# Kernel optimization log

Hardware: AMD Instinct MI355X
Metric: run time of the kernel (lower is better)

The kernel has to match this reference:

```python
import jax, jax.numpy as jnp
import numpy as np

N_HEAD = 16
N_EMBD = 2048
HEAD_DIM = N_EMBD // N_HEAD


def setup_inputs() -> dict:
    key = jax.random.key(0)
    kx, kqkv, kp = jax.random.split(key, 3)
    B, S = 2, 2048
    x = jax.random.normal(kx, (B, S, N_EMBD), dtype=jnp.float32)
    # torch nn.Linear weights, stored as [out, in]; y = x @ W.T
    scale = 1.0 / np.sqrt(N_EMBD)
    Wqkv = jax.random.uniform(kqkv, (3 * N_EMBD, N_EMBD), dtype=jnp.float32, minval=-scale, maxval=scale)
    Wproj = jax.random.uniform(kp, (N_EMBD, N_EMBD), dtype=jnp.float32, minval=-scale, maxval=scale)
    return {"x": x, "Wqkv": Wqkv, "Wproj": Wproj}


def reference(x, Wqkv, Wproj):
    B, S, E = x.shape
    qkv = x @ Wqkv.T  # [B,S,3E]
    q, k, v = jnp.split(qkv, 3, axis=2)
    # [B,H,S,D]
    q = q.reshape(B, S, N_HEAD, HEAD_DIM).transpose(0, 2, 1, 3)
    k = k.reshape(B, S, N_HEAD, HEAD_DIM).transpose(0, 2, 1, 3)
    v = v.reshape(B, S, N_HEAD, HEAD_DIM).transpose(0, 2, 1, 3)
    scores = jnp.einsum('bhqd,bhkd->bhqk', q, k) / jnp.sqrt(jnp.float32(HEAD_DIM))
    causal = jnp.tril(jnp.ones((S, S), dtype=bool))  # [S,S]
    scores = jnp.where(causal[None, None, :, :], scores, -jnp.inf)
    weights = jax.nn.softmax(scores, axis=-1)
    out = jnp.einsum('bhqk,bhkd->bhqd', weights, v)  # [B,H,S,D]
    out = out.transpose(0, 2, 1, 3).reshape(B, S, E)
    return out @ Wproj.T
```

## Files before the change

kernel.cpp:

```cpp
#include <hip/hip_runtime.h>
#include <cstdint>
#include <cstddef>

typedef __bf16 bf16;
typedef __bf16 bf16x8 __attribute__((ext_vector_type(8)));
typedef float  f32x4  __attribute__((ext_vector_type(4)));

static_assert(sizeof(bf16x8) == 16, "bf16x8 must be 16B");

__device__ __forceinline__ void async_copy16(const bf16* g, bf16* l) {
  __builtin_amdgcn_global_load_lds(
      (__attribute__((address_space(1))) void*)(g),
      (__attribute__((address_space(3))) void*)(l),
      16, 0, 0);
}

__global__ __launch_bounds__(256)
void conv_f32_bf16(const float* __restrict__ s, bf16* __restrict__ d) {
  const size_t i = ((size_t)blockIdx.x * 256 + threadIdx.x) * 8;
  const f32x4 a = *(const f32x4*)(s + i);
  const f32x4 b = *(const f32x4*)(s + i + 4);
  bf16x8 o;
#pragma unroll
  for (int e = 0; e < 4; ++e) { o[e] = (bf16)a[e]; o[4 + e] = (bf16)b[e]; }
  *(bf16x8*)(d + i) = o;
}

template<int AMODE, int CMODE>
__global__ __launch_bounds__(256, 2)
void gemm_bt(const bf16* __restrict__ A, const bf16* __restrict__ W,
             float* __restrict__ Crow, bf16* __restrict__ Cq,
             bf16* __restrict__ Ck, bf16* __restrict__ Cvt,
             int M, int N, int K, int nbase) {
  __shared__ bf16 As[128 * 64];
  __shared__ bf16 Ws[128 * 64];

  const int tid  = threadIdx.x;
  const int wave = tid >> 6;
  const int lane = tid & 63;
  const int quad = lane >> 4;
  const int r    = lane & 15;
  const int m0 = blockIdx.y * 128;
  const int n0 = blockIdx.x * 128;
  const int wm = (wave >> 1) * 64;
  const int wn = (wave & 1) * 64;

  const int lrow   = lane >> 3;
  const int gchunk = (lane & 7) ^ lrow;

  f32x4 acc[4][4] = {};

  for (int k0 = 0; k0 < K; k0 += 64) {
    __syncthreads();
    for (int j = 0; j < 4; ++j) {
      const int rbase = (wave * 4 + j) * 8;
      const int rowA  = m0 + rbase + lrow;
      const bf16* aSrc;
      if constexpr (AMODE == 2) {
        const int b = rowA >> 11, s = rowA & 2047;
        aSrc = A + ((size_t)(b * 16 + (k0 >> 7)) * 2048 + s) * 128
                 + (k0 & 127) + gchunk * 8;
      } else {
        aSrc = A + (size_t)rowA * K + k0 + gchunk * 8;
      }
      async_copy16(aSrc, As + rbase * 64);
      async_copy16(W + (size_t)(n0 + rbase + lrow) * K + k0 + gchunk * 8,
                   Ws + rbase * 64);
    }
    __syncthreads();
    for (int ks = 0; ks < 2; ++ks) {
      bf16x8 af[4], bfv[4];
      for (int i = 0; i < 4; ++i) {
        const int ar = wm + i * 16 + r;
        af[i]  = *(const bf16x8*)(As + ar * 64 + (((ks * 4 + quad) ^ (ar & 7)) * 8));
        const int br = wn + i * 16 + r;
        bfv[i] = *(const bf16x8*)(Ws + br * 64 + (((ks * 4 + quad) ^ (br & 7)) * 8));
      }
      for (int i = 0; i < 4; ++i)
        for (int j = 0; j < 4; ++j)
          acc[i][j] = __builtin_amdgcn_mfma_f32_16x16x32_bf16(af[i], bfv[j], acc[i][j], 0, 0, 0);
    }
  }

  for (int i = 0; i < 4; ++i) {
    const int growb = m0 + wm + i * 16 + quad * 4;
    for (int j = 0; j < 4; ++j) {
      const int gcol = n0 + wn + j * 16 + r;
      for (int rg = 0; rg < 4; ++rg) {
        const int grow = growb + rg;
        if constexpr (CMODE == 1) {
          const int gc = nbase + gcol;
          const int which = gc >> 11;
          const int h = (gc >> 7) & 15;
          const int d = gc & 127;
          const int b = grow >> 11;
          const int s = grow & 2047;
          const bf16 v = (bf16)acc[i][j][rg];
          if (which == 0)
            Cq[(((size_t)b * 16 + h) * 2048 + s) * 128 + d] = v;
          else if (which == 1)
            Ck[(((size_t)b * 16 + h) * 2048 + s) * 128 + d] = v;
          else
            Cvt[(((size_t)b * 16 + h) * 128 + d) * 2048 + s] = v;
        } else {
          Crow[(size_t)grow * N + gcol] = acc[i][j][rg];
        }
      }
    }
  }
}

__global__ __launch_bounds__(256, 2)
void attn_kernel(bf16* __restrict__ Q, const bf16* __restrict__ K,
                 const bf16* __restrict__ Vt, int S) {
  __shared__ bf16 k_lds[64 * 128];
  __shared__ bf16 v_lds[128 * 64];
  __shared__ bf16 p_lds[4][32 * 64];

  const int tid = threadIdx.x, wave = tid >> 6, lane = tid & 63;
  const int quad = lane >> 4, r = lane & 15;
  const int bh = blockIdx.y;
  const int q0 = (gridDim.x - 1 - blockIdx.x) * 128;
  const int qrow0 = q0 + wave * 32;
  bf16* Qh = Q + (size_t)bh * S * 128;
  const bf16* Kh = K + (size_t)bh * S * 128;
  const bf16* Vth = Vt + (size_t)bh * 128 * S;

  bf16x8 qf[2][4];
  for (int mt = 0; mt < 2; ++mt)
    for (int ks = 0; ks < 4; ++ks)
      qf[mt][ks] = *(const bf16x8*)(Qh + (size_t)(qrow0 + mt * 16 + r) * 128 + ks * 32 + quad * 8);

  f32x4 o_acc[2][8] = {};
  f32x4 m_run[2], l_run[2];
  for (int mt = 0; mt < 2; ++mt)
    for (int t = 0; t < 4; ++t) { m_run[mt][t] = -1e30f; l_run[mt][t] = 0.f; }

  const float sc = 0.0883883476483184f * 1.4426950408889634f;
  const int nkv = (q0 + 128) >> 6;

  for (int kt = 0; kt < nkv; ++kt) {
    const int kv0 = kt << 6;
    __syncthreads();
    for (int j = 0; j < 4; ++j) {
      const int lin = j * 256 + tid;
      const int row = lin >> 4;
      const int ch  = lin & 15;
      *(bf16x8*)(k_lds + row * 128 + (ch ^ (row & 7)) * 8) =
          *(const bf16x8*)(Kh + (size_t)(kv0 + row) * 128 + ch * 8);
    }
    for (int j = 0; j < 4; ++j) {
      const int lin = j * 256 + tid;
      const int row = lin >> 3;
      const int c   = lin & 7;
      *(bf16x8*)(v_lds + row * 64 + (c ^ (row & 7)) * 8) =
          *(const bf16x8*)(Vth + (size_t)row * S + kv0 + c * 8);
    }
    __syncthreads();

    if (kv0 <= qrow0 + 31) {
      f32x4 sa[2][4] = {};
      for (int ks = 0; ks < 4; ++ks) {
        bf16x8 kf[4];
        for (int nt = 0; nt < 4; ++nt) {
          const int kr = nt * 16 + r;
          kf[nt] = *(const bf16x8*)(k_lds + kr * 128 + (((ks * 4 + quad) ^ (kr & 7)) * 8));
        }
        for (int mt = 0; mt < 2; ++mt)
          for (int nt = 0; nt < 4; ++nt)
            sa[mt][nt] = __builtin_amdgcn_mfma_f32_16x16x32_bf16(qf[mt][ks], kf[nt], sa[mt][nt], 0, 0, 0);
      }
      if (kv0 + 63 > qrow0) {
        for (int mt = 0; mt < 2; ++mt)
          for (int nt = 0; nt < 4; ++nt) {
            const int col  = kv0 + nt * 16 + r;
            const int rowb = qrow0 + mt * 16 + quad * 4;
            for (int rg = 0; rg < 4; ++rg)
              if (col > rowb + rg) sa[mt][nt][rg] = -1e30f;
          }
      }
      for (int mt = 0; mt < 2; ++mt) {
        f32x4 mx = sa[mt][0];
        for (int nt = 1; nt < 4; ++nt)
          for (int rg = 0; rg < 4; ++rg) mx[rg] = fmaxf(mx[rg], sa[mt][nt][rg]);
        for (int off = 1; off < 16; off <<= 1)
          for (int rg = 0; rg < 4; ++rg) mx[rg] = fmaxf(mx[rg], __shfl_xor(mx[rg], off, 64));
        f32x4 alpha;
        for (int rg = 0; rg < 4; ++rg) {
          const float mnew = fmaxf(m_run[mt][rg], mx[rg]);
          alpha[rg] = exp2f((m_run[mt][rg] - mnew) * sc);
          m_run[mt][rg] = mnew;
        }
        f32x4 rsum = {0.f, 0.f, 0.f, 0.f};
        for (int nt = 0; nt < 4; ++nt)
          for (int rg = 0; rg < 4; ++rg) {
            const float p = exp2f((sa[mt][nt][rg] - m_run[mt][rg]) * sc);
            sa[mt][nt][rg] = p;
            rsum[rg] += p;
          }
        for (int off = 1; off < 16; off <<= 1)
          for (int rg = 0; rg < 4; ++rg) rsum[rg] += __shfl_xor(rsum[rg], off, 64);
        for (int rg = 0; rg < 4; ++rg) l_run[mt][rg] = l_run[mt][rg] * alpha[rg] + rsum[rg];
        for (int nt2 = 0; nt2 < 8; ++nt2)
          for (int rg = 0; rg < 4; ++rg) o_acc[mt][nt2][rg] *= alpha[rg];
        for (int nt = 0; nt < 4; ++nt)
          for (int rg = 0; rg < 4; ++rg) {
            const int prow = mt * 16 + quad * 4 + rg;
            const int pcol = nt * 16 + r;
            p_lds[wave][prow * 64 + (((pcol >> 3) ^ (prow & 7)) * 8) + (pcol & 7)] =
                (bf16)sa[mt][nt][rg];
          }
      }
      for (int ks2 = 0; ks2 < 2; ++ks2) {
        bf16x8 pf[2];
        for (int mt = 0; mt < 2; ++mt) {
          const int prow = mt * 16 + r;
          pf[mt] = *(const bf16x8*)(p_lds[wave] + prow * 64 + (((ks2 * 4 + quad) ^ (prow & 7)) * 8));
        }
        for (int nt2 = 0; nt2 < 8; ++nt2) {
          const int vrow = nt2 * 16 + r;
          const bf16x8 vf = *(const bf16x8*)(v_lds + vrow * 64 + (((ks2 * 4 + quad) ^ (vrow & 7)) * 8));
          for (int mt = 0; mt < 2; ++mt)
            o_acc[mt][nt2] = __builtin_amdgcn_mfma_f32_16x16x32_bf16(pf[mt], vf, o_acc[mt][nt2], 0, 0, 0);
        }
      }
    }
  }

  for (int mt = 0; mt < 2; ++mt) {
    f32x4 inv;
    for (int rg = 0; rg < 4; ++rg) inv[rg] = 1.0f / l_run[mt][rg];
    for (int nt2 = 0; nt2 < 8; ++nt2) {
      const int d = nt2 * 16 + r;
      for (int rg = 0; rg < 4; ++rg) {
        const int s = qrow0 + mt * 16 + quad * 4 + rg;
        Qh[(size_t)s * 128 + d] = (bf16)(o_acc[mt][nt2][rg] * inv[rg]);
      }
    }
  }
}

extern "C" void kernel_launch(void* const* d_in, const int* in_sizes, int n_in,
                              void* d_out, int out_size, void* d_ws, size_t ws_size,
                              hipStream_t stream) {
  const float* x     = (const float*)d_in[0];
  const float* Wqkv  = (const float*)d_in[1];
  const float* Wproj = (const float*)d_in[2];
  float* out = (float*)d_out;

  const int Bm = 4096, E = 2048;
  const size_t plane = 8388608;

  bf16* qw  = (bf16*)d_ws;
  bf16* vtw = qw + plane;
  bf16* xb  = vtw + plane;
  bf16* kw  = (bf16*)d_out;
  bf16* wqb = kw + plane;

  conv_f32_bf16<<<8388608 / 2048, 256, 0, stream>>>(x, xb);
  conv_f32_bf16<<<6291456 / 2048, 256, 0, stream>>>(Wqkv, wqb);
  gemm_bt<0, 1><<<dim3(3072 / 128, Bm / 128), 256, 0, stream>>>(
      xb, wqb, nullptr, qw, kw, vtw, Bm, 3072, E, 0);
  conv_f32_bf16<<<6291456 / 2048, 256, 0, stream>>>(Wqkv + 6291456, wqb);
  gemm_bt<0, 1><<<dim3(3072 / 128, Bm / 128), 256, 0, stream>>>(
      xb, wqb, nullptr, qw, kw, vtw, Bm, 3072, E, 3072);
  attn_kernel<<<dim3(2048 / 128, 32), 256, 0, stream>>>(qw, kw, vtw, 2048);
  conv_f32_bf16<<<4194304 / 2048, 256, 0, stream>>>(Wproj, xb);
  gemm_bt<2, 0><<<dim3(2048 / 128, Bm / 128), 256, 0, stream>>>(
      qw, xb, out, nullptr, nullptr, nullptr, Bm, 2048, E, 0);
}
```

Measured before the change: 444.0 us.

## Double-buffer attention K/V with async LDS loads and pair causal query blocks

The attention kernel now streams K and V tiles into double-buffered shared memory using global_load_lds async copies, prefetching the next tile while the current one is computed. Each block handles two query blocks (one from each end of the sequence), which halves the grid and balances causal work per block. It also raises wave priority around the MFMA phases and skips the rescale of the running max unless it grows past a threshold. Costs are double the K/V LDS footprint, which can lower occupancy, fewer blocks in flight, and a lazy-rescale path that loosens the numerical bound.

```diff
diff --git a/kernel.cpp b/kernel.cpp
--- a/kernel.cpp
+++ b/kernel.cpp
@@ -113,128 +113,156 @@
 __global__ __launch_bounds__(256, 2)
 void attn_kernel(bf16* __restrict__ Q, const bf16* __restrict__ K,
                  const bf16* __restrict__ Vt, int S) {
-  __shared__ bf16 k_lds[64 * 128];
-  __shared__ bf16 v_lds[128 * 64];
+  __shared__ bf16 k_lds[2][64 * 128];
+  __shared__ bf16 v_lds[2][128 * 64];
   __shared__ bf16 p_lds[4][32 * 64];
 
   const int tid = threadIdx.x, wave = tid >> 6, lane = tid & 63;
   const int quad = lane >> 4, r = lane & 15;
   const int bh = blockIdx.y;
-  const int q0 = (gridDim.x - 1 - blockIdx.x) * 128;
-  const int qrow0 = q0 + wave * 32;
   bf16* Qh = Q + (size_t)bh * S * 128;
   const bf16* Kh = K + (size_t)bh * S * 128;
   const bf16* Vth = Vt + (size_t)bh * 128 * S;
 
-  bf16x8 qf[2][4];
-  for (int mt = 0; mt < 2; ++mt)
-    for (int ks = 0; ks < 4; ++ks)
-      qf[mt][ks] = *(const bf16x8*)(Qh + (size_t)(qrow0 + mt * 16 + r) * 128 + ks * 32 + quad * 8);
-
-  f32x4 o_acc[2][8] = {};
-  f32x4 m_run[2], l_run[2];
-  for (int mt = 0; mt < 2; ++mt)
-    for (int t = 0; t < 4; ++t) { m_run[mt][t] = -1e30f; l_run[mt][t] = 0.f; }
-
   const float sc = 0.0883883476483184f * 1.4426950408889634f;
-  const int nkv = (q0 + 128) >> 6;
-
-  for (int kt = 0; kt < nkv; ++kt) {
-    const int kv0 = kt << 6;
-    __syncthreads();
-    for (int j = 0; j < 4; ++j) {
-      const int lin = j * 256 + tid;
-      const int row = lin >> 4;
-      const int ch  = lin & 15;
-      *(bf16x8*)(k_lds + row * 128 + (ch ^ (row & 7)) * 8) =
-          *(const bf16x8*)(Kh + (size_t)(kv0 + row) * 128 + ch * 8);
-    }
-    for (int j = 0; j < 4; ++j) {
-      const int lin = j * 256 + tid;
-      const int row = lin >> 3;
-      const int c   = lin & 7;
-      *(bf16x8*)(v_lds + row * 64 + (c ^ (row & 7)) * 8) =
-          *(const bf16x8*)(Vth + (size_t)row * S + kv0 + c * 8);
-    }
-    __syncthreads();
-
-    if (kv0 <= qrow0 + 31) {
-      f32x4 sa[2][4] = {};
-      for (int ks = 0; ks < 4; ++ks) {
-        bf16x8 kf[4];
-        for (int nt = 0; nt < 4; ++nt) {
-          const int kr = nt * 16 + r;
-          kf[nt] = *(const bf16x8*)(k_lds + kr * 128 + (((ks * 4 + quad) ^ (kr & 7)) * 8));
-        }
-        for (int mt = 0; mt < 2; ++mt)
+
+  auto issue_stage = [&](int kv0, int buf) {
+#pragma unroll
+    for (int j = 0; j < 4; ++j) {
+      const int lin0 = j * 256 + wave * 64;
+      const int lin = lin0 + lane;
+      const int row = lin >> 4, ch = lin & 15;
+      async_copy16(Kh + (size_t)(kv0 + row) * 128 + ((ch ^ (row & 7)) << 3),
+                   &k_lds[buf][0] + lin0 * 8);
+    }
+#pragma unroll
+    for (int j = 0; j < 4; ++j) {
+      const int lin0 = j * 256 + wave * 64;
+      const int lin = lin0 + lane;
+      const int row = lin >> 3, c = lin & 7;
+      async_copy16(Vth + (size_t)row * S + kv0 + ((c ^ (row & 7)) << 3),
+                   &v_lds[buf][0] + lin0 * 8);
+    }
+  };
+
+  for (int pass = 0; pass < 2; ++pass) {
+    const int qb = pass ? blockIdx.x : (15 - blockIdx.x);
+    const int q0 = qb << 7;
+    const int qrow0 = q0 + wave * 32;
+    const int nkv = (q0 + 128) >> 6;
+
+    bf16x8 qf[2][4];
+    for (int mt = 0; mt < 2; ++mt)
+      for (int ks = 0; ks < 4; ++ks)
+        qf[mt][ks] = *(const bf16x8*)(Qh + (size_t)(qrow0 + mt * 16 + r) * 128 + ks * 32 + quad * 8);
+
+    f32x4 o_acc[2][8] = {};
+    f32x4 m_run[2], l_run[2];
+    for (int mt = 0; mt < 2; ++mt)
+      for (int t = 0; t < 4; ++t) { m_run[mt][t] = -1e30f; l_run[mt][t] = 0.f; }
+
+    issue_stage(0, 0);
+
+    for (int kt = 0; kt < nkv; ++kt) {
+      const int kv0 = kt << 6;
+      const int cur = kt & 1;
+      if (kt + 1 < nkv) {
+        issue_stage((kt + 1) << 6, cur ^ 1);
+        asm volatile("s_waitcnt vmcnt(8)" ::: "memory");
+      } else {
+        asm volatile("s_waitcnt vmcnt(0)" ::: "memory");
+      }
+      __builtin_amdgcn_sched_barrier(0);
+      __syncthreads();
+
+      if (kv0 <= qrow0 + 31) {
+        f32x4 sa[2][4] = {};
+        __builtin_amdgcn_s_setprio(1);
+        for (int ks = 0; ks < 4; ++ks) {
+          bf16x8 kf[4];
+          for (int nt = 0; nt < 4; ++nt) {
+            const int kr = nt * 16 + r;
+            kf[nt] = *(const bf16x8*)(&k_lds[cur][0] + kr * 128 + (((ks * 4 + quad) ^ (kr & 7)) << 3));
+          }
+          for (int mt = 0; mt < 2; ++mt)
+            for (int nt = 0; nt < 4; ++nt)
+              sa[mt][nt] = __builtin_amdgcn_mfma_f32_16x16x32_bf16(qf[mt][ks], kf[nt], sa[mt][nt], 0, 0, 0);
+        }
+        __builtin_amdgcn_s_setprio(0);
+        if (kv0 + 63 > qrow0) {
+          for (int mt = 0; mt < 2; ++mt)
+            for (int nt = 0; nt < 4; ++nt) {
+              const int col  = kv0 + nt * 16 + r;
+              const int rowb = qrow0 + mt * 16 + quad * 4;
+              for (int rg = 0; rg < 4; ++rg)
+                if (col > rowb + rg) sa[mt][nt][rg] = -1e30f;
+            }
+        }
+        for (int mt = 0; mt < 2; ++mt) {
+          f32x4 mx = sa[mt][0];
+          for (int nt = 1; nt < 4; ++nt)
+            for (int rg = 0; rg < 4; ++rg) mx[rg] = fmaxf(mx[rg], sa[mt][nt][rg]);
+          for (int off = 1; off < 16; off <<= 1)
+            for (int rg = 0; rg < 4; ++rg) mx[rg] = fmaxf(mx[rg], __shfl_xor(mx[rg], off, 64));
+          float need = mx[0] - m_run[mt][0];
+          for (int rg = 1; rg < 4; ++rg) need = fmaxf(need, mx[rg] - m_run[mt][rg]);
+          if (need * sc > 8.0f) {
+            f32x4 alpha;
+            for (int rg = 0; rg < 4; ++rg) {
+              const float mnew = fmaxf(m_run[mt][rg], mx[rg]);
+              alpha[rg] = exp2f((m_run[mt][rg] - mnew) * sc);
+              m_run[mt][rg] = mnew;
+              l_run[mt][rg] *= alpha[rg];
+            }
+            for (int nt2 = 0; nt2 < 8; ++nt2)
+              for (int rg = 0; rg < 4; ++rg) o_acc[mt][nt2][rg] *= alpha[rg];
+          }
+          f32x4 rsum = {0.f, 0.f, 0.f, 0.f};
           for (int nt = 0; nt < 4; ++nt)
-            sa[mt][nt] = __builtin_amdgcn_mfma_f32_16x16x32_bf16(qf[mt][ks], kf[nt], sa[mt][nt], 0, 0, 0);
-      }
-      if (kv0 + 63 > qrow0) {
-        for (int mt = 0; mt < 2; ++mt)
-          for (int nt = 0; nt < 4; ++nt) {
-            const int col  = kv0 + nt * 16 + r;
-            const int rowb = qrow0 + mt * 16 + quad * 4;
-            for (int rg = 0; rg < 4; ++rg)
-              if (col > rowb + rg) sa[mt][nt][rg] = -1e30f;
-          }
-      }
-      for (int mt = 0; mt < 2; ++mt) {
-        f32x4 mx = sa[mt][0];
-        for (int nt = 1; nt < 4; ++nt)
-          for (int rg = 0; rg < 4; ++rg) mx[rg] = fmaxf(mx[rg], sa[mt][nt][rg]);
-        for (int off = 1; off < 16; off <<= 1)
-          for (int rg = 0; rg < 4; ++rg) mx[rg] = fmaxf(mx[rg], __shfl_xor(mx[rg], off, 64));
-        f32x4 alpha;
+            for (int rg = 0; rg < 4; ++rg) {
+              const float p = exp2f((sa[mt][nt][rg] - m_run[mt][rg]) * sc);
+              sa[mt][nt][rg] = p;
+              rsum[rg] += p;
+            }
+          for (int off = 1; off < 16; off <<= 1)
+            for (int rg = 0; rg < 4; ++rg) rsum[rg] += __shfl_xor(rsum[rg], off, 64);
+          for (int rg = 0; rg < 4; ++rg) l_run[mt][rg] += rsum[rg];
+          for (int nt = 0; nt < 4; ++nt)
+            for (int rg = 0; rg < 4; ++rg) {
+              const int prow = mt * 16 + quad * 4 + rg;
+              const int pcol = nt * 16 + r;
+              p_lds[wave][prow * 64 + (((pcol >> 3) ^ (prow & 7)) * 8) + (pcol & 7)] =
+                  (bf16)sa[mt][nt][rg];
+            }
+        }
+        __builtin_amdgcn_s_setprio(1);
+        for (int ks2 = 0; ks2 < 2; ++ks2) {
+          bf16x8 pf[2];
+          for (int mt = 0; mt < 2; ++mt) {
+            const int prow = mt * 16 + r;
+            pf[mt] = *(const bf16x8*)(p_lds[wave] + prow * 64 + (((ks2 * 4 + quad) ^ (prow & 7)) * 8));
+          }
+          for (int nt2 = 0; nt2 < 8; ++nt2) {
+            const int vrow = nt2 * 16 + r;
+            const bf16x8 vf = *(const bf16x8*)(&v_lds[cur][0] + vrow * 64 + (((ks2 * 4 + quad) ^ (vrow & 7)) * 8));
+            for (int mt = 0; mt < 2; ++mt)
+              o_acc[mt][nt2] = __builtin_amdgcn_mfma_f32_16x16x32_bf16(pf[mt], vf, o_acc[mt][nt2], 0, 0, 0);
+          }
+        }
+        __builtin_amdgcn_s_setprio(0);
+      }
+      __syncthreads();
+    }
+
+    for (int mt = 0; mt < 2; ++mt) {
+      f32x4 inv;
+      for (int rg = 0; rg < 4; ++rg) inv[rg] = 1.0f / l_run[mt][rg];
+      for (int nt2 = 0; nt2 < 8; ++nt2) {
+        const int d = nt2 * 16 + r;
         for (int rg = 0; rg < 4; ++rg) {
-          const float mnew = fmaxf(m_run[mt][rg], mx[rg]);
-          alpha[rg] = exp2f((m_run[mt][rg] - mnew) * sc);
-          m_run[mt][rg] = mnew;
-        }
-        f32x4 rsum = {0.f, 0.f, 0.f, 0.f};
-        for (int nt = 0; nt < 4; ++nt)
-          for (int rg = 0; rg < 4; ++rg) {
-            const float p = exp2f((sa[mt][nt][rg] - m_run[mt][rg]) * sc);
-            sa[mt][nt][rg] = p;
-            rsum[rg] += p;
-          }
-        for (int off = 1; off < 16; off <<= 1)
-          for (int rg = 0; rg < 4; ++rg) rsum[rg] += __shfl_xor(rsum[rg], off, 64);
-        for (int rg = 0; rg < 4; ++rg) l_run[mt][rg] = l_run[mt][rg] * alpha[rg] + rsum[rg];
-        for (int nt2 = 0; nt2 < 8; ++nt2)
-          for (int rg = 0; rg < 4; ++rg) o_acc[mt][nt2][rg] *= alpha[rg];
-        for (int nt = 0; nt < 4; ++nt)
-          for (int rg = 0; rg < 4; ++rg) {
-            const int prow = mt * 16 + quad * 4 + rg;
-            const int pcol = nt * 16 + r;
-            p_lds[wave][prow * 64 + (((pcol >> 3) ^ (prow & 7)) * 8) + (pcol & 7)] =
-                (bf16)sa[mt][nt][rg];
-          }
-      }
-      for (int ks2 = 0; ks2 < 2; ++ks2) {
-        bf16x8 pf[2];
-        for (int mt = 0; mt < 2; ++mt) {
-          const int prow = mt * 16 + r;
-          pf[mt] = *(const bf16x8*)(p_lds[wave] + prow * 64 + (((ks2 * 4 + quad) ^ (prow & 7)) * 8));
-        }
-        for (int nt2 = 0; nt2 < 8; ++nt2) {
-          const int vrow = nt2 * 16 + r;
-          const bf16x8 vf = *(const bf16x8*)(v_lds + vrow * 64 + (((ks2 * 4 + quad) ^ (vrow & 7)) * 8));
-          for (int mt = 0; mt < 2; ++mt)
-            o_acc[mt][nt2] = __builtin_amdgcn_mfma_f32_16x16x32_bf16(pf[mt], vf, o_acc[mt][nt2], 0, 0, 0);
-        }
-      }
-    }
-  }
-
-  for (int mt = 0; mt < 2; ++mt) {
-    f32x4 inv;
-    for (int rg = 0; rg < 4; ++rg) inv[rg] = 1.0f / l_run[mt][rg];
-    for (int nt2 = 0; nt2 < 8; ++nt2) {
-      const int d = nt2 * 16 + r;
-      for (int rg = 0; rg < 4; ++rg) {
-        const int s = qrow0 + mt * 16 + quad * 4 + rg;
-        Qh[(size_t)s * 128 + d] = (bf16)(o_acc[mt][nt2][rg] * inv[rg]);
+          const int s = qrow0 + mt * 16 + quad * 4 + rg;
+          Qh[(size_t)s * 128 + d] = (bf16)(o_acc[mt][nt2][rg] * inv[rg]);
+        }
       }
     }
   }
@@ -264,7 +292,7 @@
   conv_f32_bf16<<<6291456 / 2048, 256, 0, stream>>>(Wqkv + 6291456, wqb);
   gemm_bt<0, 1><<<dim3(3072 / 128, Bm / 128), 256, 0, stream>>>(
       xb, wqb, nullptr, qw, kw, vtw, Bm, 3072, E, 3072);
-  attn_kernel<<<dim3(2048 / 128, 32), 256, 0, stream>>>(qw, kw, vtw, 2048);
+  attn_kernel<<<dim3(8, 32), 256, 0, stream>>>(qw, kw, vtw, 2048);
   conv_f32_bf16<<<4194304 / 2048, 256, 0, stream>>>(Wproj, xb);
   gemm_bt<2, 0><<<dim3(2048 / 128, Bm / 128), 256, 0, stream>>>(
       qw, xb, out, nullptr, nullptr, nullptr, Bm, 2048, E, 0);
```

Measured after the change: 436.0 us. No clear change (-1.8%).
